# Optimization experiments

Hardware: AMD Instinct MI355X
Metric: run time of the kernel (lower is better)

Reference implementation:

```python
import jax, jax.numpy as jnp
import numpy as np

B, H, W, C = 2, 64, 64, 512
GROUPS = 32
EPS = 1e-5


def group_norm(x, gamma, beta):
    b, h, w, c = x.shape
    xg = x.reshape(b, h, w, GROUPS, c // GROUPS)
    mu = xg.mean(axis=(1, 2, 4), keepdims=True)
    var = xg.var(axis=(1, 2, 4), keepdims=True)
    xn = ((xg - mu) * jax.lax.rsqrt(var + EPS)).reshape(b, h, w, c)
    return xn * gamma + beta


def setup_inputs() -> dict:
    key = jax.random.key(0)
    ks = jax.random.split(key, 12)
    wscale = 0.02
    inputs = jax.random.normal(ks[0], (B, H, W, C), jnp.float32)
    gamma = jnp.ones((C,), jnp.float32)
    beta = jnp.zeros((C,), jnp.float32)
    Wq = jax.random.normal(ks[1], (C, C), jnp.float32) * wscale
    bq = jnp.zeros((C,), jnp.float32)
    Wk = jax.random.normal(ks[2], (C, C), jnp.float32) * wscale
    bk = jnp.zeros((C,), jnp.float32)
    Wv = jax.random.normal(ks[3], (C, C), jnp.float32) * wscale
    bv = jnp.zeros((C,), jnp.float32)
    Wp = jax.random.normal(ks[4], (C, C), jnp.float32) * wscale
    bp = jnp.zeros((C,), jnp.float32)
    return {"inputs": inputs, "gamma": gamma, "beta": beta,
            "Wq": Wq, "bq": bq, "Wk": Wk, "bk": bk,
            "Wv": Wv, "bv": bv, "Wp": Wp, "bp": bp}


def reference(inputs, gamma, beta, Wq, bq, Wk, bk, Wv, bv, Wp, bp):
    b, h, w, c = inputs.shape
    x = group_norm(inputs, gamma, beta)
    # QKV projections on [b, h, w, c], flatten spatial to sequence hw
    q = (x @ Wq + bq).reshape(b, h * w, c)
    k = (x @ Wk + bk).reshape(b, h * w, c)
    v = (x @ Wv + bv).reshape(b, h * w, c)
    scale = 1.0 / jnp.sqrt(jnp.asarray(c, q.dtype))
    # y[b,i,j] = <q_i, k_j> / sqrt(c); softmax over keys j (last axis, keras default)
    attn = jax.nn.softmax(jnp.einsum('bqc,bkc->bqk', q, k) * scale, axis=-1)
    # out_i = sum_j attn[i,j] * v_j  (matches v @ y^T in the original)
    o = jnp.einsum('bqk,bkc->bqc', attn, v).reshape(b, h, w, c)
    return (o @ Wp + bp) + inputs
```

## Files before the change

### kernel.cpp

```cpp
#include <hip/hip_runtime.h>
#include <hip/hip_bf16.h>
#include <cstddef>


typedef __bf16 bf16;
typedef __attribute__((ext_vector_type(8))) __bf16 bf16x8;
typedef __attribute__((ext_vector_type(4))) __bf16 bf16x4;
typedef __attribute__((ext_vector_type(4))) float f32x4;

#define SEQ   4096
#define CCH   512
#define NBAT  2
#define NOMASK 0x7FFFFFFF
#define SMEM_BYTES 32768
#define PGRID 1024

__device__ __forceinline__ void grid_bar(unsigned* bar, int idx) {
    __syncthreads();
    if (threadIdx.x == 0) {
        __threadfence();
        __hip_atomic_fetch_add(&bar[idx], 1u, __ATOMIC_RELEASE,
                               __HIP_MEMORY_SCOPE_AGENT);
        while (__hip_atomic_load(&bar[idx], __ATOMIC_RELAXED,
                                 __HIP_MEMORY_SCOPE_AGENT) < (unsigned)PGRID)
            __builtin_amdgcn_s_sleep(1);
        __threadfence();
    }
    __syncthreads();
}

__device__ __forceinline__ void prep_unit(
    char* smem, int bid, const float* __restrict__ x,
    const float* __restrict__ Wq, const float* __restrict__ Wk,
    const float* __restrict__ Wv, const float* __restrict__ Wp,
    const float* __restrict__ bq, const float* __restrict__ bk,
    const float* __restrict__ bv,
    float* __restrict__ statsP, bf16* __restrict__ WqkvT,
    bf16* __restrict__ WpT, float* __restrict__ biasQKV) {
    const int tid = threadIdx.x;
    if (bid < 512) {
        float* red = (float*)smem;
        int bg = bid >> 3, c = bid & 7;
        int b = bg >> 5, g = bg & 31;
        const float* base = x + (size_t)b * SEQ * CCH + g * 16;
        float s = 0.f, ss = 0.f;
        for (int i = tid; i < 2048; i += 256) {
            int sp = c * 512 + (i >> 2), q = i & 3;
            float4 v = *(const float4*)(base + (size_t)sp * CCH + q * 4);
            s  += v.x + v.y + v.z + v.w;
            ss += v.x * v.x + v.y * v.y + v.z * v.z + v.w * v.w;
        }
        #pragma unroll
        for (int o = 32; o > 0; o >>= 1) { s += __shfl_down(s, o); ss += __shfl_down(ss, o); }
        int wave = tid >> 6, lane = tid & 63;
        if (lane == 0) { red[wave] = s; red[4 + wave] = ss; }
        __syncthreads();
        if (tid == 0) {
            statsP[bg * 16 + c]     = red[0] + red[1] + red[2] + red[3];
            statsP[bg * 16 + 8 + c] = red[4] + red[5] + red[6] + red[7];
        }
        __syncthreads();
    } else if (bid < 1536) {
        float (*tile)[33] = (float(*)[33])smem;
        int w = bid - 512;
        int z = w >> 8, rest = w & 255;
        int k0 = (rest >> 4) * 32, n0 = (rest & 15) * 32;
        const float* W = (z == 0) ? Wq : (z == 1) ? Wk : (z == 2) ? Wv : Wp;
        int tx = tid & 31, ty = tid >> 5;
        #pragma unroll
        for (int i = ty; i < 32; i += 8)
            tile[i][tx] = W[(size_t)(k0 + i) * CCH + n0 + tx];
        __syncthreads();
        bf16* dst = (z < 3) ? (WqkvT + (size_t)z * CCH * CCH) : WpT;
        #pragma unroll
        for (int i = ty; i < 32; i += 8)
            dst[(size_t)(n0 + i) * CCH + k0 + tx] = (bf16)tile[tx][i];
        __syncthreads();
    } else {
        for (int i = tid; i < 1536; i += 256) {
            float v = (i < 512) ? bq[i] : (i < 1024) ? bk[i - 512] : bv[i - 1024];
            biasQKV[i] = v;
        }
    }
}

__device__ __forceinline__ void gn_table(char* smem, const float* __restrict__ statsP) {
    float* tbl = (float*)smem;
    const int tid = threadIdx.x;
    if (tid < 64) {
        float S = 0.f, SS = 0.f;
        #pragma unroll
        for (int c = 0; c < 8; ++c) { S += statsP[tid * 16 + c]; SS += statsP[tid * 16 + 8 + c]; }
        float mu = S * (1.f / 65536.f);
        float rs = rsqrtf(SS * (1.f / 65536.f) - mu * mu + 1e-5f);
        tbl[tid * 2] = mu; tbl[tid * 2 + 1] = rs;
    }
    __syncthreads();
}

__device__ __forceinline__ void gn_unit(
    char* smem, int w, const float* __restrict__ x,
    const float* __restrict__ gamma, const float* __restrict__ beta,
    bf16* __restrict__ xn) {
    const float* tbl = (const float*)smem;
    size_t idx = (size_t)w * 256 + threadIdx.x;
    int c4 = (int)(idx & 127);
    int b = (int)(idx >> 19);
    int bg = b * 32 + (c4 >> 2);
    float mu = tbl[bg * 2], rs = tbl[bg * 2 + 1];
    float4 v  = ((const float4*)x)[idx];
    float4 gm = ((const float4*)gamma)[c4];
    float4 bt = ((const float4*)beta)[c4];
    bf16x4 o;
    o[0] = (bf16)((v.x - mu) * rs * gm.x + bt.x);
    o[1] = (bf16)((v.y - mu) * rs * gm.y + bt.y);
    o[2] = (bf16)((v.z - mu) * rs * gm.z + bt.z);
    o[3] = (bf16)((v.w - mu) * rs * gm.w + bt.w);
    ((bf16x4*)xn)[idx] = o;
}

__device__ __forceinline__ void vtrans_unit(char* smem,
                                            const bf16* __restrict__ qkv,
                                            bf16* __restrict__ vT,
                                            int b, int s0, int c0) {
    bf16 (*tile)[65] = (bf16(*)[65])smem;
    const int tx = threadIdx.x & 63;
    const int w = threadIdx.x >> 6;
    #pragma unroll
    for (int i = 0; i < 16; ++i) {
        int row = w + i * 4;
        tile[row][tx] = qkv[((size_t)b * SEQ + s0 + row) * 1536 + 1024 + c0 + tx];
    }
    __syncthreads();
    #pragma unroll
    for (int i = 0; i < 16; ++i) {
        int row = w + i * 4;
        vT[((size_t)b * CCH + c0 + row) * SEQ + s0 + tx] = tile[tx][row];
    }
    __syncthreads();
}

template <int EPI, int BN>
__device__ __forceinline__ void gemm2_body(
    char* smem, int bxi, int byi, int bzi,
    const bf16* __restrict__ A, long long aBatch, int lda,
    const bf16* __restrict__ Bt, long long bBatch, int ldb,
    void* __restrict__ Cout, long long cBatch, int ldc,
    int K, int bkmask, float scale,
    const float* __restrict__ bias, const float* __restrict__ resid,
    float* __restrict__ lsum, long long lsumBatch) {
    constexpr int JN = BN / 32;
    bf16* As = (bf16*)smem;
    bf16* Bs = (bf16*)(smem + 16384);
    const int tid = threadIdx.x;
    const int lane = tid & 63;
    const int wave = tid >> 6;

    int zb = bzi, kc = 0;
    if constexpr (EPI == 2) { kc = zb & 1; zb >>= 1; }
    const long long m0 = (long long)bxi * 128;
    const long long n0 = (long long)byi * BN;
    const bf16* Ab = A + (long long)zb * aBatch + (EPI == 2 ? (long long)kc * 2048 : 0);
    const bf16* Bb = Bt + (long long)zb * bBatch + (EPI == 2 ? (long long)kc * 2048 : 0);

    const int wm = (wave & 1) * 64;
    const int wn = (wave >> 1) * (BN / 2);
    const int fm = lane & 15;
    const int q4 = lane >> 4;

    f32x4 acc[4][JN];
    #pragma unroll
    for (int i = 0; i < 4; ++i)
        #pragma unroll
        for (int j = 0; j < JN; ++j)
            acc[i][j] = (f32x4){0.f, 0.f, 0.f, 0.f};

    const int srow = tid >> 3;
    const int schunk = (tid & 7) ^ (srow & 7);

    for (int k0 = 0; k0 < K; k0 += 64) {
        const int kA = k0 + schunk * 8;
        const int kB = (k0 & bkmask) + schunk * 8;
        #pragma unroll
        for (int cb = 0; cb < 4; ++cb) {
            const bf16* g = Ab + (m0 + cb * 32 + srow) * (long long)lda + kA;
            __builtin_amdgcn_global_load_lds((const __attribute__((address_space(1))) void*)g,
                                             (__attribute__((address_space(3))) void*)&As[cb * 2048 + tid * 8], 16, 0, 0);
        }
        #pragma unroll
        for (int cb = 0; cb < BN / 32; ++cb) {
            const bf16* g = Bb + (n0 + cb * 32 + srow) * (long long)ldb + kB;
            __builtin_amdgcn_global_load_lds((const __attribute__((address_space(1))) void*)g,
                                             (__attribute__((address_space(3))) void*)&Bs[cb * 2048 + tid * 8], 16, 0, 0);
        }
        __syncthreads();
        #pragma unroll
        for (int kcc = 0; kcc < 2; ++kcc) {
            bf16x8 fa[4], fb[JN];
            #pragma unroll
            for (int i = 0; i < 4; ++i) {
                const int row = wm + i * 16 + fm;
                const int sw = ((kcc * 4 + q4) ^ (fm & 7)) * 8;
                fa[i] = *(const bf16x8*)&As[row * 64 + sw];
            }
            #pragma unroll
            for (int j = 0; j < JN; ++j) {
                const int row = wn + j * 16 + fm;
                const int sw = ((kcc * 4 + q4) ^ (fm & 7)) * 8;
                fb[j] = *(const bf16x8*)&Bs[row * 64 + sw];
            }
            #pragma unroll
            for (int i = 0; i < 4; ++i)
                #pragma unroll
                for (int j = 0; j < JN; ++j)
                    acc[i][j] = __builtin_amdgcn_mfma_f32_16x16x32_bf16(fa[i], fb[j], acc[i][j], 0, 0, 0);
        }
        __syncthreads();
    }

    float* lrow = (float*)(smem + 1024);
    if constexpr (EPI == 2) {
        float* lscr = (float*)smem;
        const float* lsb = lsum + (long long)zb * lsumBatch + m0;
        const int row = tid & 127, h = tid >> 7;
        float s = 0.f;
        #pragma unroll
        for (int p = 0; p < 32; ++p)
            s += lsb[(long long)(h * 32 + p) * SEQ + row];
        lscr[tid] = s;
        __syncthreads();
        if (tid < 128) lrow[tid] = 1.f / (lscr[tid] + lscr[tid + 128]);
        __syncthreads();
    }

    const int col = lane & 15;
    const int rowb = (lane >> 4) * 4;

    if constexpr (EPI == 1) {
        bf16* Pb = (bf16*)Cout + (long long)zb * cBatch;
        float* lsw = lsum + (long long)zb * lsumBatch
                   + ((long long)byi * 2 + (wave >> 1)) * SEQ;
        #pragma unroll
        for (int i = 0; i < 4; ++i) {
            float rs[4] = {0.f, 0.f, 0.f, 0.f};
            long long mg = m0 + wm + i * 16 + rowb;
            #pragma unroll
            for (int j = 0; j < JN; ++j) {
                long long ng = n0 + wn + j * 16 + col;
                #pragma unroll
                for (int r = 0; r < 4; ++r) {
                    float e = __expf(acc[i][j][r] * scale);
                    rs[r] += e;
                    Pb[(mg + r) * (long long)ldc + ng] = (bf16)e;
                }
            }
            #pragma unroll
            for (int r = 0; r < 4; ++r) {
                rs[r] += __shfl_xor(rs[r], 1);
                rs[r] += __shfl_xor(rs[r], 2);
                rs[r] += __shfl_xor(rs[r], 4);
                rs[r] += __shfl_xor(rs[r], 8);
            }
            if (col == 0) {
                #pragma unroll
                for (int r = 0; r < 4; ++r) lsw[mg + r] = rs[r];
            }
        }
    } else {
        #pragma unroll
        for (int i = 0; i < 4; ++i) {
            #pragma unroll
            for (int j = 0; j < JN; ++j) {
                long long mg = m0 + wm + i * 16 + rowb;
                long long ng = n0 + wn + j * 16 + col;
                #pragma unroll
                for (int r = 0; r < 4; ++r) {
                    float v = acc[i][j][r];
                    long long m = mg + r;
                    if constexpr (EPI == 0) {
                        ((bf16*)Cout)[m * (long long)ldc + ng] = (bf16)(v + bias[ng]);
                    } else if constexpr (EPI == 2) {
                        float inv = lrow[(int)(m - m0)];
                        ((bf16*)Cout)[(long long)zb * cBatch + m * (long long)ldc
                                      + kc * 512 + ng] = (bf16)(v * inv);
                    } else {
                        ((float*)Cout)[m * (long long)ldc + ng] =
                            v + bias[ng] + resid[m * CCH + ng];
                    }
                }
            }
        }
    }
}

struct FusedArgs {
    const float *x, *gamma, *beta, *Wq, *bq, *Wk, *bk, *Wv, *bv, *Wp, *bp;
    float* out;
    float* statsP; float* biasQKV; bf16* WqkvT; bf16* WpT; bf16* xn;
    float* lsum; bf16* qkv; bf16* o2; bf16* vT; bf16* P;
    unsigned* bar;
};

__global__ __launch_bounds__(256, 4) void persistent(FusedArgs a) {
    __shared__ __align__(16) char smem[SMEM_BYTES];
    const int nb = PGRID;
    const float scale = 0.044194173824159216f;

    for (int w = blockIdx.x; w < 1537; w += nb)
        prep_unit(smem, w, a.x, a.Wq, a.Wk, a.Wv, a.Wp, a.bq, a.bk, a.bv,
                  a.statsP, a.WqkvT, a.WpT, a.biasQKV);
    grid_bar(a.bar, 0);

    gn_table(smem, a.statsP);
    for (int w = blockIdx.x; w < 4096; w += nb)
        gn_unit(smem, w, a.x, a.gamma, a.beta, a.xn);
    grid_bar(a.bar, 1);

    for (int w = blockIdx.x; w < 768; w += nb) {
        int l = w >> 3;
        gemm2_body<0, 128>(smem, (w & 7) * 8 + l / 12, l % 12, 0,
                           a.xn, 0, CCH, a.WqkvT, 0, CCH, a.qkv, 0, 1536,
                           CCH, NOMASK, 1.f, a.biasQKV, nullptr, nullptr, 0);
    }
    grid_bar(a.bar, 2);

    for (int w = blockIdx.x; w < 3072; w += nb) {
        if (w < 1024) {
            int b = w >> 9, r = w & 511;
            vtrans_unit(smem, a.qkv, a.vT, b, (r >> 3) * 64, (r & 7) * 64);
        } else {
            int u = w - 1024;
            int bz = u >> 10, r = u & 1023;
            int l = r >> 3;
            gemm2_body<1, 128>(smem, (r & 7) * 4 + (l >> 5), l & 31, bz,
                               a.qkv, (long long)SEQ * 1536, 1536,
                               a.qkv + 512, (long long)SEQ * 1536, 1536,
                               a.P, (long long)SEQ * SEQ, SEQ,
                               CCH, NOMASK, scale, nullptr, nullptr,
                               a.lsum, 64LL * SEQ);
        }
    }
    grid_bar(a.bar, 3);

    for (int w = blockIdx.x; w < 1024; w += nb) {
        int l = w >> 3;
        int S = (w & 7) * 16 + (l >> 3);
        gemm2_body<2, 64>(smem, S & 31, l & 7, S >> 5,
                          a.P, (long long)SEQ * SEQ, SEQ,
                          a.vT, (long long)CCH * SEQ, SEQ,
                          a.o2, (long long)SEQ * 1024, 1024,
                          2048, NOMASK, 1.f, nullptr, nullptr,
                          a.lsum, 64LL * SEQ);
    }
    grid_bar(a.bar, 4);

    for (int w = blockIdx.x; w < 512; w += nb) {
        int l = w >> 3;
        gemm2_body<3, 64>(smem, (w & 7) * 8 + (l >> 3), l & 7, 0,
                          a.o2, 0, 1024, a.WpT, 0, CCH, a.out, 0, CCH,
                          1024, 511, 1.f, a.bp, a.x, nullptr, 0);
    }
}

__global__ __launch_bounds__(256) void k_prep(
    const float* x, const float* Wq, const float* Wk, const float* Wv,
    const float* Wp, const float* bq, const float* bk, const float* bv,
    float* statsP, bf16* WqkvT, bf16* WpT, float* biasQKV) {
    __shared__ __align__(16) char smem[4352];
    prep_unit(smem, blockIdx.x, x, Wq, Wk, Wv, Wp, bq, bk, bv,
              statsP, WqkvT, WpT, biasQKV);
}

__global__ __launch_bounds__(256) void k_gn(
    const float* x, const float* statsP, const float* gamma,
    const float* beta, bf16* xn) {
    __shared__ __align__(16) char smem[512];
    gn_table(smem, statsP);
    gn_unit(smem, blockIdx.x, x, statsP == nullptr ? gamma : gamma, beta, xn);
}

template <int EPI, int BN>
__global__ __launch_bounds__(256, 2) void k_gemm2(
    const bf16* A, long long aBatch, int lda,
    const bf16* Bt, long long bBatch, int ldb,
    void* Cout, long long cBatch, int ldc,
    int K, int bkmask, float scale,
    const float* bias, const float* resid,
    float* lsum, long long lsumBatch) {
    __shared__ __align__(16) char smem[SMEM_BYTES];
    gemm2_body<EPI, BN>(smem, blockIdx.x, blockIdx.y, blockIdx.z,
                        A, aBatch, lda, Bt, bBatch, ldb, Cout, cBatch, ldc,
                        K, bkmask, scale, bias, resid, lsum, lsumBatch);
}

__global__ __launch_bounds__(256, 2) void k_qk_vtrans(
    const bf16* qkv, bf16* vT, bf16* P, float* lsum, float scale,
    int vtBlocks, long long qkBatch, long long pBatch, long long lsumBatch) {
    __shared__ __align__(16) char smem[SMEM_BYTES];
    const int bid = blockIdx.x;
    if (bid < vtBlocks) {
        int b = bid >> 9, r = bid & 511;
        vtrans_unit(smem, qkv, vT, b, (r >> 3) * 64, (r & 7) * 64);
    } else {
        int q = bid - vtBlocks;
        int bz = q >> 10, r = q & 1023;
        gemm2_body<1, 128>(smem, r >> 5, r & 31, bz,
                           qkv, qkBatch, 1536, qkv + 512, qkBatch, 1536,
                           P, pBatch, SEQ, CCH, NOMASK, scale,
                           nullptr, nullptr, lsum, lsumBatch);
    }
}

extern "C" void kernel_launch(void* const* d_in, const int* in_sizes, int n_in,
                              void* d_out, int out_size, void* d_ws, size_t ws_size,
                              hipStream_t stream) {
    const float* x     = (const float*)d_in[0];
    const float* gamma = (const float*)d_in[1];
    const float* beta  = (const float*)d_in[2];
    const float* Wq    = (const float*)d_in[3];
    const float* bq    = (const float*)d_in[4];
    const float* Wk    = (const float*)d_in[5];
    const float* bk    = (const float*)d_in[6];
    const float* Wv    = (const float*)d_in[7];
    const float* bv    = (const float*)d_in[8];
    const float* Wp    = (const float*)d_in[9];
    const float* bp    = (const float*)d_in[10];
    float* out = (float*)d_out;

    constexpr size_t OFF_STATS = 0;
    constexpr size_t OFF_BIAS  = 4096;
    constexpr size_t OFF_BAR   = 10240;
    constexpr size_t OFF_WQKVT = 12288;
    constexpr size_t OFF_WPT   = 1585152;
    constexpr size_t OFF_XN    = 2109440;
    constexpr size_t OFF_LSUM  = OFF_XN;
    constexpr size_t OFF_QKV   = 10498048;
    constexpr size_t OFF_O2    = OFF_QKV;
    constexpr size_t OFF_VT    = 35663872;
    constexpr size_t OFF_P     = 44052480;
    constexpr size_t NEED_FULL = OFF_P + (size_t)NBAT * SEQ * SEQ * 2;

    char* ws = (char*)d_ws;
    float* statsP  = (float*)(ws + OFF_STATS);
    float* biasQKV = (float*)(ws + OFF_BIAS);
    unsigned* bar  = (unsigned*)(ws + OFF_BAR);
    bf16*  WqkvT   = (bf16*)(ws + OFF_WQKVT);
    bf16*  WpT     = (bf16*)(ws + OFF_WPT);
    bf16*  xn      = (bf16*)(ws + OFF_XN);
    float* lsum    = (float*)(ws + OFF_LSUM);
    bf16*  qkv     = (bf16*)(ws + OFF_QKV);
    bf16*  o2      = (bf16*)(ws + OFF_O2);
    bf16*  vT      = (bf16*)(ws + OFF_VT);
    bf16*  P       = (bf16*)(ws + OFF_P);

    const float scale = 0.044194173824159216f;
    const bool full = ws_size >= NEED_FULL;

    bool usePersist = false;
    if (full) {
        int occ = 0;
        hipError_t oe = hipOccupancyMaxActiveBlocksPerMultiprocessor(
            &occ, (const void*)persistent, 256, 0);
        usePersist = (oe == hipSuccess && occ >= 4);
        if (!usePersist) (void)hipGetLastError();
    }

    if (usePersist) {
        hipMemsetAsync(ws + OFF_BAR, 0, 64, stream);
        FusedArgs a{x, gamma, beta, Wq, bq, Wk, bk, Wv, bv, Wp, bp, out,
                    statsP, biasQKV, WqkvT, WpT, xn, lsum, qkv, o2, vT, P, bar};
        persistent<<<PGRID, 256, 0, stream>>>(a);
    } else {
        k_prep<<<1537, 256, 0, stream>>>(x, Wq, Wk, Wv, Wp, bq, bk, bv,
                                         statsP, WqkvT, WpT, biasQKV);
        k_gn<<<4096, 256, 0, stream>>>(x, statsP, gamma, beta, xn);
        k_gemm2<0, 128><<<dim3(64, 12, 1), 256, 0, stream>>>(
            xn, 0, CCH, WqkvT, 0, CCH, qkv, 0, 1536,
            CCH, NOMASK, 1.f, biasQKV, nullptr, nullptr, 0);
        if (full) {
            k_qk_vtrans<<<3072, 256, 0, stream>>>(
                qkv, vT, P, lsum, scale, 1024,
                (long long)SEQ * 1536, (long long)SEQ * SEQ, 64LL * SEQ);
            k_gemm2<2, 128><<<dim3(32, 4, NBAT * 2), 256, 0, stream>>>(
                P, (long long)SEQ * SEQ, SEQ, vT, (long long)CCH * SEQ, SEQ,
                o2, (long long)SEQ * 1024, 1024,
                2048, NOMASK, 1.f, nullptr, nullptr, lsum, 64LL * SEQ);
        } else {
            for (int b = 0; b < NBAT; ++b) {
                const bf16* qb = qkv + (long long)b * SEQ * 1536;
                k_qk_vtrans<<<1536, 256, 0, stream>>>(
                    qb, vT + (long long)b * CCH * SEQ, P,
                    lsum + (long long)b * 64 * SEQ, scale, 512, 0, 0, 0);
                k_gemm2<2, 128><<<dim3(32, 4, 2), 256, 0, stream>>>(
                    P, 0, SEQ, vT + (long long)b * CCH * SEQ, 0, SEQ,
                    o2 + (long long)b * SEQ * 1024, 0, 1024,
                    2048, NOMASK, 1.f, nullptr, nullptr,
                    lsum + (long long)b * 64 * SEQ, 0);
            }
        }
        k_gemm2<3, 64><<<dim3(64, 8, 1), 256, 0, stream>>>(
            o2, 0, 1024, WpT, 0, CCH, out, 0, CCH,
            1024, 511, 1.f, bp, x, nullptr, 0);
    }
}
```

Measured before the change: 212.0 us.

## Replace persistent grid-barrier kernel with per-stage launches and swizzled block mapping

New measurement: 227.6 us. 1.07x slower.

```diff
diff --git a/kernel.cpp b/kernel.cpp
--- a/kernel.cpp
+++ b/kernel.cpp
@@ -376,7 +376,58 @@
     const float* beta, bf16* xn) {
     __shared__ __align__(16) char smem[512];
     gn_table(smem, statsP);
-    gn_unit(smem, blockIdx.x, x, statsP == nullptr ? gamma : gamma, beta, xn);
+    gn_unit(smem, blockIdx.x, x, gamma, beta, xn);
+}
+
+__global__ __launch_bounds__(256, 2) void k_qkv_m(
+    const bf16* xn, const bf16* WqkvT, bf16* qkv, const float* biasQKV) {
+    __shared__ __align__(16) char smem[SMEM_BYTES];
+    int w = blockIdx.x, l = w >> 3;
+    gemm2_body<0, 128>(smem, (w & 7) * 8 + l / 12, l % 12, 0,
+                       xn, 0, CCH, WqkvT, 0, CCH, qkv, 0, 1536,
+                       CCH, NOMASK, 1.f, biasQKV, nullptr, nullptr, 0);
+}
+
+__global__ __launch_bounds__(256, 2) void k_vtrans_m(const bf16* qkv, bf16* vT) {
+    __shared__ __align__(16) char smem[8448];
+    int w = blockIdx.x, b = w >> 9, r = w & 511;
+    vtrans_unit(smem, qkv, vT, b, (r >> 3) * 64, (r & 7) * 64);
+}
+
+__global__ __launch_bounds__(256, 2) void k_qk_m(
+    const bf16* qkv, bf16* P, float* lsum, float scale) {
+    __shared__ __align__(16) char smem[SMEM_BYTES];
+    int w = blockIdx.x;
+    int bz = w >> 10, r = w & 1023, l = r >> 3;
+    gemm2_body<1, 128>(smem, (r & 7) * 4 + (l >> 5), l & 31, bz,
+                       qkv, (long long)SEQ * 1536, 1536,
+                       qkv + 512, (long long)SEQ * 1536, 1536,
+                       P, (long long)SEQ * SEQ, SEQ,
+                       CCH, NOMASK, scale, nullptr, nullptr,
+                       lsum, 64LL * SEQ);
+}
+
+__global__ __launch_bounds__(256, 2) void k_pv_m(
+    const bf16* P, const bf16* vT, bf16* o2, float* lsum) {
+    __shared__ __align__(16) char smem[SMEM_BYTES];
+    int w = blockIdx.x, l = w >> 3;
+    int S = (w & 7) * 16 + (l >> 3);
+    gemm2_body<2, 64>(smem, S & 31, l & 7, S >> 5,
+                      P, (long long)SEQ * SEQ, SEQ,
+                      vT, (long long)CCH * SEQ, SEQ,
+                      o2, (long long)SEQ * 1024, 1024,
+                      2048, NOMASK, 1.f, nullptr, nullptr,
+                      lsum, 64LL * SEQ);
+}
+
+__global__ __launch_bounds__(256, 2) void k_proj_m(
+    const bf16* o2, const bf16* WpT, float* out, const float* bp,
+    const float* x) {
+    __shared__ __align__(16) char smem[SMEM_BYTES];
+    int w = blockIdx.x, l = w >> 3;
+    gemm2_body<3, 64>(smem, (w & 7) * 8 + (l >> 3), l & 7, 0,
+                      o2, 0, 1024, WpT, 0, CCH, out, 0, CCH,
+                      1024, 511, 1.f, bp, x, nullptr, 0);
 }
 
 template <int EPI, int BN>
@@ -443,7 +494,6 @@
     char* ws = (char*)d_ws;
     float* statsP  = (float*)(ws + OFF_STATS);
     float* biasQKV = (float*)(ws + OFF_BIAS);
-    unsigned* bar  = (unsigned*)(ws + OFF_BAR);
     bf16*  WqkvT   = (bf16*)(ws + OFF_WQKVT);
     bf16*  WpT     = (bf16*)(ws + OFF_WPT);
     bf16*  xn      = (bf16*)(ws + OFF_XN);
@@ -456,20 +506,15 @@
     const float scale = 0.044194173824159216f;
     const bool full = ws_size >= NEED_FULL;
 
-    bool usePersist = false;
     if (full) {
-        int occ = 0;
-        hipError_t oe = hipOccupancyMaxActiveBlocksPerMultiprocessor(
-            &occ, (const void*)persistent, 256, 0);
-        usePersist = (oe == hipSuccess && occ >= 4);
-        if (!usePersist) (void)hipGetLastError();
-    }
-
-    if (usePersist) {
-        hipMemsetAsync(ws + OFF_BAR, 0, 64, stream);
-        FusedArgs a{x, gamma, beta, Wq, bq, Wk, bk, Wv, bv, Wp, bp, out,
-                    statsP, biasQKV, WqkvT, WpT, xn, lsum, qkv, o2, vT, P, bar};
-        persistent<<<PGRID, 256, 0, stream>>>(a);
+        k_prep<<<1537, 256, 0, stream>>>(x, Wq, Wk, Wv, Wp, bq, bk, bv,
+                                         statsP, WqkvT, WpT, biasQKV);
+        k_gn<<<4096, 256, 0, stream>>>(x, statsP, gamma, beta, xn);
+        k_qkv_m<<<768, 256, 0, stream>>>(xn, WqkvT, qkv, biasQKV);
+        k_vtrans_m<<<1024, 256, 0, stream>>>(qkv, vT);
+        k_qk_m<<<2048, 256, 0, stream>>>(qkv, P, lsum, scale);
+        k_pv_m<<<1024, 256, 0, stream>>>(P, vT, o2, lsum);
+        k_proj_m<<<512, 256, 0, stream>>>(o2, WpT, out, bp, x);
     } else {
         k_prep<<<1537, 256, 0, stream>>>(x, Wq, Wk, Wv, Wp, bq, bk, bv,
                                          statsP, WqkvT, WpT, biasQKV);
@@ -477,26 +522,16 @@
         k_gemm2<0, 128><<<dim3(64, 12, 1), 256, 0, stream>>>(
             xn, 0, CCH, WqkvT, 0, CCH, qkv, 0, 1536,
             CCH, NOMASK, 1.f, biasQKV, nullptr, nullptr, 0);
-        if (full) {
-            k_qk_vtrans<<<3072, 256, 0, stream>>>(
-                qkv, vT, P, lsum, scale, 1024,
-                (long long)SEQ * 1536, (long long)SEQ * SEQ, 64LL * SEQ);
-            k_gemm2<2, 128><<<dim3(32, 4, NBAT * 2), 256, 0, stream>>>(
-                P, (long long)SEQ * SEQ, SEQ, vT, (long long)CCH * SEQ, SEQ,
-                o2, (long long)SEQ * 1024, 1024,
-                2048, NOMASK, 1.f, nullptr, nullptr, lsum, 64LL * SEQ);
-        } else {
-            for (int b = 0; b < NBAT; ++b) {
-                const bf16* qb = qkv + (long long)b * SEQ * 1536;
-                k_qk_vtrans<<<1536, 256, 0, stream>>>(
-                    qb, vT + (long long)b * CCH * SEQ, P,
-                    lsum + (long long)b * 64 * SEQ, scale, 512, 0, 0, 0);
-                k_gemm2<2, 128><<<dim3(32, 4, 2), 256, 0, stream>>>(
-                    P, 0, SEQ, vT + (long long)b * CCH * SEQ, 0, SEQ,
-                    o2 + (long long)b * SEQ * 1024, 0, 1024,
-                    2048, NOMASK, 1.f, nullptr, nullptr,
-                    lsum + (long long)b * 64 * SEQ, 0);
-            }
+        for (int b = 0; b < NBAT; ++b) {
+            const bf16* qb = qkv + (long long)b * SEQ * 1536;
+            k_qk_vtrans<<<1536, 256, 0, stream>>>(
+                qb, vT + (long long)b * CCH * SEQ, P,
+                lsum + (long long)b * 64 * SEQ, scale, 512, 0, 0, 0);
+            k_gemm2<2, 128><<<dim3(32, 4, 2), 256, 0, stream>>>(
+                P, 0, SEQ, vT + (long long)b * CCH * SEQ, 0, SEQ,
+                o2 + (long long)b * SEQ * 1024, 0, 1024,
+                2048, NOMASK, 1.f, nullptr, nullptr,
+                lsum + (long long)b * 64 * SEQ, 0);
         }
         k_gemm2<3, 64><<<dim3(64, 8, 1), 256, 0, stream>>>(
             o2, 0, 1024, WpT, 0, CCH, out, 0, CCH,
```
